# Kernel tuning notes

Measured on AMD Instinct MI355X. Metric: run time of the kernel, lower is better.

Reference implementation:

```python
import jax, jax.numpy as jnp
import numpy as np

NUM_HEADS = 3
DIM = 96
MLP_HIDDEN = int(DIM * 4.0)
LN_EPS = 1e-5


def _layernorm(x, g, b):
    mu = jnp.mean(x, axis=-1, keepdims=True)
    var = jnp.mean(jnp.square(x - mu), axis=-1, keepdims=True)
    return (x - mu) * jax.lax.rsqrt(var + LN_EPS) * g + b


def setup_inputs() -> dict:
    key = jax.random.key(0)
    ks = jax.random.split(key, 12)
    B, H, W, T, C = 1, 48, 48, 48, DIM
    L = H * W * T
    s = 0.02
    return {
        "x": jax.random.normal(ks[0], (B, L, C), dtype=jnp.float32),
        "mask_matrix": jnp.zeros((1, 1), dtype=jnp.float32),
        "ln1_g": jnp.ones((C,), jnp.float32),
        "ln1_b": jnp.zeros((C,), jnp.float32),
        "qkv_w": jax.random.normal(ks[1], (3 * C, C), jnp.float32) * s,
        "qkv_b": jnp.zeros((3 * C,), jnp.float32),
        "proj_w": jax.random.normal(ks[2], (C, C), jnp.float32) * s,
        "proj_b": jnp.zeros((C,), jnp.float32),
        "ln2_g": jnp.ones((C,), jnp.float32),
        "ln2_b": jnp.zeros((C,), jnp.float32),
        "fc1_w": jax.random.normal(ks[3], (MLP_HIDDEN, C), jnp.float32) * s,
        "fc1_b": jnp.zeros((MLP_HIDDEN,), jnp.float32),
        "fc2_w": jax.random.normal(ks[4], (C, MLP_HIDDEN), jnp.float32) * s,
        "fc2_b": jnp.zeros((C,), jnp.float32),
        "H": 48, "W": 48, "T": 48,
    }


def reference(x, mask_matrix, ln1_g, ln1_b, qkv_w, qkv_b, proj_w, proj_b,
              ln2_g, ln2_b, fc1_w, fc1_b, fc2_w, fc2_b, H, W, T):
    B, L, C = x.shape
    nh = NUM_HEADS
    hd = C // nh
    scale = hd ** -0.5

    shortcut = x
    h = _layernorm(x, ln1_g, ln1_b)
    # [B,H,W,T,C] -> permute(0,3,1,2,4) -> [B*T, H*W, C]  (axial_dims='12', extra_dim=3)
    h = h.reshape(B, H, W, T, C).transpose(0, 3, 1, 2, 4).reshape(B * T, H * W, C)
    B_, N, _ = h.shape

    qkv = h @ qkv_w.T + qkv_b                       # [B_, N, 3C]
    # faithful to torch: permute(1,0,2) -> reshape(1,N,3,nh,B_*hd) -> permute(2,0,3,1,4)
    qkv = jnp.transpose(qkv, (1, 0, 2)).reshape(1, N, 3, nh, B_ * hd)
    qkv = jnp.transpose(qkv, (2, 0, 3, 1, 4))       # [3, 1, nh, N, B_*hd]
    q, k, v = qkv[0] * scale, qkv[1], qkv[2]

    attn = jax.nn.softmax(q @ jnp.swapaxes(k, -2, -1), axis=-1)  # [1, nh, N, N]
    o = attn @ v                                    # [1, nh, N, B_*hd]
    o = jnp.transpose(o, (0, 2, 1, 3)).reshape(B_, N, C)
    o = o @ proj_w.T + proj_b
    # faithful to torch: plain view back to [B, H*W*T, C] (no inverse permute)
    o = o.reshape(B, H * W * T, C)

    x = shortcut + o
    h2 = _layernorm(x, ln2_g, ln2_b)
    m = jax.nn.gelu(h2 @ fc1_w.T + fc1_b, approximate=False) @ fc2_w.T + fc2_b
    return x + m
```

## Files before the change

### kernel.cpp

```cpp
#include <hip/hip_runtime.h>
#include <hip/hip_bf16.h>
#include <math.h>

typedef __bf16 bf16_t;
typedef __bf16 bf16x8 __attribute__((ext_vector_type(8)));
typedef __bf16 bf16x4 __attribute__((ext_vector_type(4)));
typedef float f32x4 __attribute__((ext_vector_type(4)));

#define AS1q __attribute__((address_space(1)))
#define AS3q __attribute__((address_space(3)))

__device__ __forceinline__ void gload_lds16(const bf16_t* g, bf16_t* l) {
    __builtin_amdgcn_global_load_lds((AS1q void*)g, (AS3q void*)l, 16, 0, 0);
}

#define LROWS   110592
#define CDIM    96
#define NTOK    2304
#define FDIM    1536
#define YSTR    3538944ll
#define SSTR    5308416ll
#define SCALE_Q 0.1767766952966369f

__device__ __forceinline__ float gelu_f(float v) {
    float xs = v * 0.70710678118654752f;
    float a  = fabsf(xs);
    float t  = __builtin_amdgcn_rcpf(fmaf(0.3275911f, a, 1.0f));
    float p  = t * fmaf(t, fmaf(t, fmaf(t, fmaf(t, 1.061405429f, -1.453152027f),
                                        1.421413741f), -0.284496736f), 0.254829592f);
    float e  = __expf(-a * a);
    float erfx = copysignf(fmaf(-p, e, 1.0f), xs);
    return 0.5f * v * (1.0f + erfx);
}

__global__ __launch_bounds__(256)
void conv_w(const float* __restrict__ a, const float* __restrict__ b,
            const float* __restrict__ c, const float* __restrict__ d,
            bf16_t* __restrict__ out)
{
    int i = blockIdx.x * 256 + threadIdx.x;
    float v;
    if (i < 27648)       v = a[i];
    else if (i < 36864)  v = b[i - 27648];
    else if (i < 73728)  v = c[i - 36864];
    else                 v = d[i - 73728];
    out[i] = (bf16_t)v;
}

__global__ __launch_bounds__(256)
void ln4_kernel(const float* __restrict__ x, const float* __restrict__ gamma,
                const float* __restrict__ beta, bf16_t* __restrict__ out, int permute)
{
    int wave = threadIdx.x >> 6;
    int half = (threadIdx.x >> 5) & 1;
    int cl   = threadIdx.x & 31;
    int row  = blockIdx.x * 8 + wave * 2 + half;
    bool act = cl < 24;
    const f32x4* xr = (const f32x4*)(x + (size_t)row * CDIM);
    f32x4 v = {0.f, 0.f, 0.f, 0.f};
    if (act) v = xr[cl];
    float s = v[0] + v[1] + v[2] + v[3];
    #pragma unroll
    for (int off = 16; off > 0; off >>= 1) s += __shfl_xor(s, off, 64);
    float mean = s * (1.f / 96.f);
    f32x4 d = {0.f, 0.f, 0.f, 0.f};
    if (act) { d[0]=v[0]-mean; d[1]=v[1]-mean; d[2]=v[2]-mean; d[3]=v[3]-mean; }
    float vs = d[0]*d[0] + d[1]*d[1] + d[2]*d[2] + d[3]*d[3];
    #pragma unroll
    for (int off = 16; off > 0; off >>= 1) vs += __shfl_xor(vs, off, 64);
    float rstd = rsqrtf(vs * (1.f / 96.f) + 1e-5f);
    size_t orow = row;
    if (permute) { int t = row % 48; int n = row / 48; orow = (size_t)t * NTOK + n; }
    if (act) {
        f32x4 g = ((const f32x4*)gamma)[cl];
        f32x4 b = ((const f32x4*)beta)[cl];
        bf16x4 o;
        #pragma unroll
        for (int j = 0; j < 4; j++) o[j] = (bf16_t)(d[j] * rstd * g[j] + b[j]);
        *(bf16x4*)(out + orow * CDIM + cl * 4) = o;
    }
}

__global__ __launch_bounds__(256)
void softmax_k(const bf16_t* __restrict__ S, bf16_t* __restrict__ P,
               long long sZ, long long pZ)
{
    int wv = threadIdx.x >> 6, lane = threadIdx.x & 63;
    int row = blockIdx.x * 4 + wv;
    const bf16_t* sr = S + (size_t)blockIdx.z * sZ + (size_t)row * NTOK;
    bf16_t* pr = P + (size_t)blockIdx.z * pZ + (size_t)row * NTOK;
    float v[36];
    float mx = -1e30f;
    #pragma unroll
    for (int t = 0; t < 9; t++) {
        bf16x4 c = *(const bf16x4*)(sr + (size_t)(t * 64 + lane) * 4);
        #pragma unroll
        for (int j = 0; j < 4; j++) { v[t*4+j] = (float)c[j]; mx = fmaxf(mx, v[t*4+j]); }
    }
    #pragma unroll
    for (int off = 32; off > 0; off >>= 1) mx = fmaxf(mx, __shfl_xor(mx, off, 64));
    float sum = 0.f;
    #pragma unroll
    for (int j = 0; j < 36; j++) { v[j] = __expf(v[j] - mx); sum += v[j]; }
    #pragma unroll
    for (int off = 32; off > 0; off >>= 1) sum += __shfl_xor(sum, off, 64);
    float inv = 1.f / sum;
    #pragma unroll
    for (int t = 0; t < 9; t++) {
        bf16x4 o;
        #pragma unroll
        for (int j = 0; j < 4; j++) o[j] = (bf16_t)(v[t*4+j] * inv);
        *(bf16x4*)(pr + (size_t)(t * 64 + lane) * 4) = o;
    }
}

template<int BN, int EPI, int NBY>
__global__ __launch_bounds__(256, 2)
void gemm_bt(const bf16_t* __restrict__ A, const bf16_t* __restrict__ W,
             void* __restrict__ out, int K,
             long long aZ, long long wZ, long long oZ, float scale)
{
    constexpr int BM = 128, BK = 64;
    constexpr int MI = 4;
    constexpr int NT = BN / 32;
    constexpr int NB = 18 * NBY;
    constexpr int CHK = (NB + 7) / 8;
    __shared__ bf16_t As[2][BM * BK];
    __shared__ bf16_t Bs[2][BN * BK];

    int id = blockIdx.x;
    int id2 = (id & 7) * CHK + (id >> 3);
    if (id2 >= NB) return;
    int p  = id2 / 108;
    int r_ = id2 - p * 108;
    int by = p * 6 + (r_ % 6);
    int bx = r_ / 6;

    const int tid = threadIdx.x;
    const int wave = tid >> 6, lane = tid & 63;
    const int quad = lane >> 4, l16 = lane & 15;
    const int wm = wave & 1, wn = wave >> 1;
    const int z = blockIdx.z;
    A += (size_t)z * aZ;
    W += (size_t)z * wZ;
    const int m0 = bx * BM, n0 = by * BN;

    f32x4 acc[MI][NT];
    #pragma unroll
    for (int i = 0; i < MI; i++)
        #pragma unroll
        for (int j = 0; j < NT; j++) { f32x4 zz = {0.f, 0.f, 0.f, 0.f}; acc[i][j] = zz; }

    const int srow = lane >> 3;
    const int scol = lane & 7;

    auto stage = [&](int buf, int k0) {
        for (int it = wave; it < BM / 8; it += 4) {
            int r = it * 8 + srow;
            int cg = scol ^ (r & 7);
            gload_lds16(A + (size_t)(m0 + r) * K + k0 + cg * 8, &As[buf][it * 512]);
        }
        for (int it = wave; it < BN / 8; it += 4) {
            int r = it * 8 + srow;
            int cg = scol ^ (r & 7);
            gload_lds16(W + (size_t)(n0 + r) * K + k0 + cg * 8, &Bs[buf][it * 512]);
        }
    };

    stage(0, 0);
    __syncthreads();

    int cur = 0;
    for (int k0 = 0; k0 < K; k0 += BK) {
        if (k0 + BK < K) stage(cur ^ 1, k0 + BK);

        bf16x8 af[MI][2], bfr[NT][2];
        #pragma unroll
        for (int i = 0; i < MI; i++) {
            int r = wm * 64 + i * 16 + l16;
            #pragma unroll
            for (int kk = 0; kk < 2; kk++)
                af[i][kk] = *(const bf16x8*)&As[cur][r * 64 + (((kk * 4 + quad) ^ (r & 7)) << 3)];
        }
        #pragma unroll
        for (int j = 0; j < NT; j++) {
            int c = wn * (BN / 2) + j * 16 + l16;
            #pragma unroll
            for (int kk = 0; kk < 2; kk++)
                bfr[j][kk] = *(const bf16x8*)&Bs[cur][c * 64 + (((kk * 4 + quad) ^ (c & 7)) << 3)];
        }
        #pragma unroll
        for (int kk = 0; kk < 2; kk++)
            #pragma unroll
            for (int i = 0; i < MI; i++)
                #pragma unroll
                for (int j = 0; j < NT; j++)
                    acc[i][j] = __builtin_amdgcn_mfma_f32_16x16x32_bf16(af[i][kk], bfr[j][kk], acc[i][j], 0, 0, 0);

        __syncthreads();
        cur ^= 1;
    }

    #pragma unroll
    for (int i = 0; i < MI; i++)
        #pragma unroll
        for (int j = 0; j < NT; j++)
            #pragma unroll
            for (int ri = 0; ri < 4; ri++) {
                int r = m0 + wm * 64 + i * 16 + quad * 4 + ri;
                int c = n0 + wn * (BN / 2) + j * 16 + l16;
                float v = acc[i][j][ri];
                if constexpr (EPI == 1) {
                    bf16_t* op = (bf16_t*)out + (size_t)z * oZ;
                    op[(size_t)r * NTOK + c] = (bf16_t)(v * scale);
                } else {
                    int b = r / 48, rr = r - b * 48;
                    ((bf16_t*)out)[((size_t)(b * NTOK + rr * 48 + z * 16)) * CDIM + c] = (bf16_t)v;
                }
            }
}

template<int N, int K, int KC, int EPI>
__global__ __launch_bounds__(256, 2)
void gemm_ws(const bf16_t* __restrict__ A, const bf16_t* __restrict__ Wg,
             void* __restrict__ out, const float* __restrict__ bias,
             const float* __restrict__ resid,
             bf16_t* __restrict__ out2, const float* __restrict__ g2,
             const float* __restrict__ b2)
{
    constexpr int KP = K + 8;
    constexpr int NT = N / 16;
    constexpr int KI = KC / 32;
    __shared__ __attribute__((aligned(16))) bf16_t Ws[N * KP];

    const int tid = threadIdx.x;
    const int wave = tid >> 6, lane = tid & 63;
    const int quad = lane >> 4, l16 = lane & 15;
    const int m0 = blockIdx.x * 256;

    constexpr int CH = N * K / 8;
    for (int c = tid; c < CH; c += 256) {
        int row = c / (K / 8), kc = c - row * (K / 8);
        bf16x8 w = *(const bf16x8*)(Wg + row * K + kc * 8);
        *(bf16x8*)(Ws + row * KP + kc * 8) = w;
    }
    __syncthreads();

    const bf16_t* Ar = A + (size_t)(m0 + wave * 64 + l16) * K + quad * 8;

    const int t = m0 / NTOK;
    const int nb = m0 - t * NTOK;

    auto epi_tile = [&](int nt, const f32x4* a4) {
        int c = nt * 16 + l16;
        if constexpr (EPI == 0) {
            int jj = t * 288 + c;
            int g = jj / FDIM, mm = jj - g * FDIM;
            float bv = bias[c];
            if (g < 6) {
                bf16_t* yp = (bf16_t*)out + (size_t)g * YSTR + mm;
                #pragma unroll
                for (int i = 0; i < 4; i++)
                    #pragma unroll
                    for (int ri = 0; ri < 4; ri++) {
                        int n = nb + wave * 64 + i * 16 + quad * 4 + ri;
                        yp[(size_t)n * FDIM] = (bf16_t)(a4[i][ri] + bv);
                    }
            } else {
                bf16_t* vp = out2 + (size_t)(g - 6) * YSTR + (size_t)mm * NTOK;
                #pragma unroll
                for (int i = 0; i < 4; i++) {
                    int n0q = nb + wave * 64 + i * 16 + quad * 4;
                    bf16x4 o;
                    #pragma unroll
                    for (int ri = 0; ri < 4; ri++) o[ri] = (bf16_t)(a4[i][ri] + bv);
                    *(bf16x4*)(vp + n0q) = o;
                }
            }
        } else {
            float bv = bias[c];
            #pragma unroll
            for (int i = 0; i < 4; i++)
                #pragma unroll
                for (int ri = 0; ri < 4; ri++) {
                    int r = m0 + wave * 64 + i * 16 + quad * 4 + ri;
                    float v = a4[i][ri] + bv;
                    if constexpr (EPI == 3) {
                        v = gelu_f(v);
                        ((bf16_t*)out)[(size_t)r * N + c] = (bf16_t)v;
                    } else {
                        ((float*)out)[(size_t)r * N + c] = v + resid[(size_t)r * N + c];
                    }
                }
        }
    };

    if constexpr (KC == K && EPI != 5) {
        bf16x8 af[4][KI];
        #pragma unroll
        for (int i = 0; i < 4; i++)
            #pragma unroll
            for (int kk = 0; kk < KI; kk++)
                af[i][kk] = *(const bf16x8*)(Ar + (size_t)i * 16 * K + kk * 32);
        #pragma unroll 2
        for (int nt = 0; nt < NT; nt++) {
            bf16x8 bfr[KI];
            #pragma unroll
            for (int kk = 0; kk < KI; kk++)
                bfr[kk] = *(const bf16x8*)(Ws + (nt * 16 + l16) * KP + kk * 32 + quad * 8);
            f32x4 a4[4];
            #pragma unroll
            for (int i = 0; i < 4; i++) { f32x4 zz = {0.f, 0.f, 0.f, 0.f}; a4[i] = zz; }
            #pragma unroll
            for (int kk = 0; kk < KI; kk++)
                #pragma unroll
                for (int i = 0; i < 4; i++)
                    a4[i] = __builtin_amdgcn_mfma_f32_16x16x32_bf16(af[i][kk], bfr[kk], a4[i], 0, 0, 0);
            epi_tile(nt, a4);
        }
    } else {
        f32x4 acc[4][NT];
        #pragma unroll
        for (int i = 0; i < 4; i++)
            #pragma unroll
            for (int j = 0; j < NT; j++) { f32x4 zz = {0.f, 0.f, 0.f, 0.f}; acc[i][j] = zz; }
        for (int kc0 = 0; kc0 < K; kc0 += KC) {
            bf16x8 af[4][KI];
            #pragma unroll
            for (int i = 0; i < 4; i++)
                #pragma unroll
                for (int kk = 0; kk < KI; kk++)
                    af[i][kk] = *(const bf16x8*)(Ar + (size_t)i * 16 * K + kc0 + kk * 32);
            #pragma unroll
            for (int nt = 0; nt < NT; nt++) {
                #pragma unroll
                for (int kk = 0; kk < KI; kk++) {
                    bf16x8 b = *(const bf16x8*)(Ws + (nt * 16 + l16) * KP + kc0 + kk * 32 + quad * 8);
                    #pragma unroll
                    for (int i = 0; i < 4; i++)
                        acc[i][nt] = __builtin_amdgcn_mfma_f32_16x16x32_bf16(af[i][kk], b, acc[i][nt], 0, 0, 0);
                }
            }
        }
        if constexpr (EPI == 5) {
            float bv[NT], gv[NT], bb[NT];
            #pragma unroll
            for (int nt = 0; nt < NT; nt++) {
                int c = nt * 16 + l16;
                bv[nt] = bias[c]; gv[nt] = g2[c]; bb[nt] = b2[c];
            }
            #pragma unroll
            for (int i = 0; i < 4; i++)
                #pragma unroll
                for (int ri = 0; ri < 4; ri++) {
                    int r = m0 + wave * 64 + i * 16 + quad * 4 + ri;
                    float u[NT];
                    float s = 0.f;
                    #pragma unroll
                    for (int nt = 0; nt < NT; nt++) {
                        int c = nt * 16 + l16;
                        u[nt] = acc[i][nt][ri] + bv[nt] + resid[(size_t)r * N + c];
                        ((float*)out)[(size_t)r * N + c] = u[nt];
                        s += u[nt];
                    }
                    #pragma unroll
                    for (int off = 8; off > 0; off >>= 1) s += __shfl_xor(s, off, 64);
                    float mean = s * (1.f / 96.f);
                    float vs = 0.f;
                    #pragma unroll
                    for (int nt = 0; nt < NT; nt++) {
                        float dd = u[nt] - mean;
                        u[nt] = dd;
                        vs += dd * dd;
                    }
                    #pragma unroll
                    for (int off = 8; off > 0; off >>= 1) vs += __shfl_xor(vs, off, 64);
                    float rstd = rsqrtf(vs * (1.f / 96.f) + 1e-5f);
                    #pragma unroll
                    for (int nt = 0; nt < NT; nt++) {
                        int c = nt * 16 + l16;
                        out2[(size_t)r * N + c] = (bf16_t)(u[nt] * rstd * gv[nt] + bb[nt]);
                    }
                }
        } else {
            #pragma unroll
            for (int nt = 0; nt < NT; nt++) {
                f32x4 a4[4];
                #pragma unroll
                for (int i = 0; i < 4; i++) a4[i] = acc[i][nt];
                epi_tile(nt, a4);
            }
        }
    }
}

__global__ __launch_bounds__(256, 4)
void mlp_fused(const bf16_t* __restrict__ A, const bf16_t* __restrict__ W1g,
               const bf16_t* __restrict__ W2g, const float* __restrict__ b1,
               const float* __restrict__ b2, const float* __restrict__ resid,
               float* __restrict__ out)
{
    constexpr int KP1 = 104;
    __shared__ __attribute__((aligned(16))) bf16_t W1c[2][32 * KP1];
    __shared__ __attribute__((aligned(16))) bf16_t W2c[2][96 * 40];
    __shared__ __attribute__((aligned(16))) bf16_t Tb[128 * 40];

    const int tid = threadIdx.x;
    const int wave = tid >> 6, lane = tid & 63;
    const int quad = lane >> 4, l16 = lane & 15;
    const int m0 = blockIdx.x * 128;

    const bf16_t* Ar = A + (size_t)(m0 + wave * 32 + l16) * 96 + quad * 8;
    bf16x8 af[2][3];
    #pragma unroll
    for (int i = 0; i < 2; i++)
        #pragma unroll
        for (int kk = 0; kk < 3; kk++)
            af[i][kk] = *(const bf16x8*)(Ar + (size_t)i * 16 * 96 + kk * 32);

    bf16x4 w1n[3], w2n[3];
    #pragma unroll
    for (int q = 0; q < 3; q++) {
        int e = q * 256 + tid;
        w1n[q] = *(const bf16x4*)(W1g + e * 4);
        int row = e >> 3, sub = e & 7;
        w2n[q] = *(const bf16x4*)(W2g + row * 384 + sub * 4);
    }
    #pragma unroll
    for (int q = 0; q < 3; q++) {
        int e = q * 256 + tid;
        int r1 = e / 24, s1 = e - r1 * 24;
        *(bf16x4*)(&W1c[0][r1 * KP1 + s1 * 4]) = w1n[q];
        int row = e >> 3, sub = e & 7;
        *(bf16x4*)(&W2c[0][row * 40 + sub * 4]) = w2n[q];
    }
    __syncthreads();

    f32x4 acc2[2][6];
    #pragma unroll
    for (int i = 0; i < 2; i++)
        #pragma unroll
        for (int j = 0; j < 6; j++) { f32x4 zz = {0.f, 0.f, 0.f, 0.f}; acc2[i][j] = zz; }

    for (int c = 0; c < 12; c++) {
        const int pb = c & 1;
        if (c < 11) {
            #pragma unroll
            for (int q = 0; q < 3; q++) {
                int e = q * 256 + tid;
                w1n[q] = *(const bf16x4*)(W1g + (c + 1) * 3072 + e * 4);
                int row = e >> 3, sub = e & 7;
                w2n[q] = *(const bf16x4*)(W2g + row * 384 + (c + 1) * 32 + sub * 4);
            }
        }
        f32x4 a1[2][2];
        #pragma unroll
        for (int i = 0; i < 2; i++)
            #pragma unroll
            for (int s = 0; s < 2; s++) { f32x4 zz = {0.f, 0.f, 0.f, 0.f}; a1[i][s] = zz; }
        #pragma unroll
        for (int s = 0; s < 2; s++) {
            int n = s * 16 + l16;
            #pragma unroll
            for (int kk = 0; kk < 3; kk++) {
                bf16x8 b = *(const bf16x8*)(&W1c[pb][n * KP1 + kk * 32 + quad * 8]);
                #pragma unroll
                for (int i = 0; i < 2; i++)
                    a1[i][s] = __builtin_amdgcn_mfma_f32_16x16x32_bf16(af[i][kk], b, a1[i][s], 0, 0, 0);
            }
        }
        #pragma unroll
        for (int s = 0; s < 2; s++) {
            int n = c * 32 + s * 16 + l16;
            float bv = b1[n];
            #pragma unroll
            for (int i = 0; i < 2; i++)
                #pragma unroll
                for (int ri = 0; ri < 4; ri++) {
                    float u = gelu_f(a1[i][s][ri] + bv);
                    Tb[(wave * 32 + i * 16 + quad * 4 + ri) * 40 + s * 16 + l16] = (bf16_t)u;
                }
        }
        if (c < 11) {
            #pragma unroll
            for (int q = 0; q < 3; q++) {
                int e = q * 256 + tid;
                int r1 = e / 24, s1 = e - r1 * 24;
                *(bf16x4*)(&W1c[pb ^ 1][r1 * KP1 + s1 * 4]) = w1n[q];
                int row = e >> 3, sub = e & 7;
                *(bf16x4*)(&W2c[pb ^ 1][row * 40 + sub * 4]) = w2n[q];
            }
        }
        bf16x8 a2[2];
        #pragma unroll
        for (int i = 0; i < 2; i++)
            a2[i] = *(const bf16x8*)(Tb + (wave * 32 + i * 16 + l16) * 40 + quad * 8);
        #pragma unroll
        for (int nt = 0; nt < 6; nt++) {
            bf16x8 b = *(const bf16x8*)(&W2c[pb][(nt * 16 + l16) * 40 + quad * 8]);
            #pragma unroll
            for (int i = 0; i < 2; i++)
                acc2[i][nt] = __builtin_amdgcn_mfma_f32_16x16x32_bf16(a2[i], b, acc2[i][nt], 0, 0, 0);
        }
        __syncthreads();
    }

    #pragma unroll
    for (int i = 0; i < 2; i++)
        #pragma unroll
        for (int nt = 0; nt < 6; nt++)
            #pragma unroll
            for (int ri = 0; ri < 4; ri++) {
                int r = m0 + wave * 32 + i * 16 + quad * 4 + ri;
                int cc = nt * 16 + l16;
                out[(size_t)r * 96 + cc] = acc2[i][nt][ri] + b2[cc] + resid[(size_t)r * 96 + cc];
            }
}

extern "C" void kernel_launch(void* const* d_in, const int* in_sizes, int n_in,
                              void* d_out, int out_size, void* d_ws, size_t ws_size,
                              hipStream_t stream)
{
    const float* x      = (const float*)d_in[0];
    const float* ln1_g  = (const float*)d_in[2];
    const float* ln1_b  = (const float*)d_in[3];
    const float* qkv_w  = (const float*)d_in[4];
    const float* qkv_b  = (const float*)d_in[5];
    const float* proj_w = (const float*)d_in[6];
    const float* proj_b = (const float*)d_in[7];
    const float* ln2_g  = (const float*)d_in[8];
    const float* ln2_b  = (const float*)d_in[9];
    const float* fc1_w  = (const float*)d_in[10];
    const float* fc1_b  = (const float*)d_in[11];
    const float* fc2_w  = (const float*)d_in[12];
    const float* fc2_b  = (const float*)d_in[13];

    const size_t SZ_WB = 110592ull * 2;
    const size_t SZ_HP = 10616832ull * 2;
    const size_t SZ_Y  = 31850496ull * 2;
    const size_t SZ_YV = 10616832ull * 2;

    char* ws = (char*)d_ws;
    size_t oWB = 0;
    size_t oHP = oWB + SZ_WB;
    size_t oY  = oHP + SZ_HP;
    size_t oYV = oY + SZ_Y;
    size_t oS  = oYV + SZ_YV;

    bf16_t* Wb    = (bf16_t*)(ws + oWB);
    bf16_t* Wqkv  = Wb;
    bf16_t* Wproj = Wb + 27648;
    bf16_t* Wfc1  = Wb + 36864;
    bf16_t* Wfc2  = Wb + 73728;
    bf16_t* hp    = (bf16_t*)(ws + oHP);
    bf16_t* Y     = (bf16_t*)(ws + oY);
    bf16_t* Yv    = (bf16_t*)(ws + oYV);
    bf16_t* Pb    = (bf16_t*)(ws + oY);
    bf16_t* Sb    = (bf16_t*)(ws + oS);
    float*  x2    = (float*)(ws + oS);
    float*  outp  = (float*)d_out;

    dim3 blk(256);

    conv_w<<<dim3(432), blk, 0, stream>>>(qkv_w, proj_w, fc1_w, fc2_w, Wb);
    ln4_kernel<<<dim3(13824), blk, 0, stream>>>(x, ln1_g, ln1_b, hp, 1);
    gemm_ws<288, 96, 96, 0><<<dim3(432), blk, 0, stream>>>(hp, Wqkv, Y, qkv_b,
                                                           nullptr, Yv, nullptr, nullptr);
    gemm_bt<128, 1, 18><<<dim3(328, 1, 3), blk, 0, stream>>>(Y, Y + 3 * YSTR, Sb,
                                                             1536, YSTR, YSTR, SSTR, SCALE_Q);
    softmax_k<<<dim3(576, 1, 3), blk, 0, stream>>>(Sb, Pb, SSTR, SSTR);
    gemm_bt<128, 2, 12><<<dim3(216, 1, 3), blk, 0, stream>>>(Pb, Yv, hp,
                                                             2304, SSTR, YSTR, 0, 0.f);
    gemm_ws<96, 96, 96, 5><<<dim3(432), blk, 0, stream>>>(hp, Wproj, x2, proj_b, x,
                                                          hp, ln2_g, ln2_b);
    mlp_fused<<<dim3(864), blk, 0, stream>>>(hp, Wfc1, Wfc2, fc1_b, fc2_b, x2, outp);
}
```

Measured before the change: 386.4 us.

## Replace attention GEMMs with 256x256-tile, 512-thread double-buffered pipelined kernel

Replaces the 128-row-tile attention GEMM (QK^T and PV) with a 256x256 tile kernel using 8 waves. Each wave now computes a 128x64 sub-tile, which raises reuse of data loaded into LDS. Global-to-LDS loads are issued two tiles ahead and tracked with explicit vmcnt waits and raw barriers, and s_setprio is raised around the MFMA section. Block IDs are remapped so that contiguous work is grouped per XCD. The larger tiles mean fewer blocks (243 and 162 in total) and heavier register use, which may reduce occupancy and leave part of the device idle.

After: 364.4 us. -5.7%, faster.

```diff
diff --git a/kernel.cpp b/kernel.cpp
--- a/kernel.cpp
+++ b/kernel.cpp
@@ -114,101 +114,122 @@
     }
 }
 
-template<int BN, int EPI, int NBY>
-__global__ __launch_bounds__(256, 2)
-void gemm_bt(const bf16_t* __restrict__ A, const bf16_t* __restrict__ W,
-             void* __restrict__ out, int K,
-             long long aZ, long long wZ, long long oZ, float scale)
-{
-    constexpr int BM = 128, BK = 64;
-    constexpr int MI = 4;
-    constexpr int NT = BN / 32;
-    constexpr int NB = 18 * NBY;
-    constexpr int CHK = (NB + 7) / 8;
-    __shared__ bf16_t As[2][BM * BK];
-    __shared__ bf16_t Bs[2][BN * BK];
-
-    int id = blockIdx.x;
-    int id2 = (id & 7) * CHK + (id >> 3);
-    if (id2 >= NB) return;
-    int p  = id2 / 108;
-    int r_ = id2 - p * 108;
-    int by = p * 6 + (r_ % 6);
-    int bx = r_ / 6;
+template<int EPI>
+__global__ __launch_bounds__(512, 1)
+void gemm_bt2(const bf16_t* __restrict__ A, const bf16_t* __restrict__ W,
+              void* __restrict__ out, int K,
+              long long aZ, long long wZ, long long oZ, float scale)
+{
+    constexpr int BM = 256, BN = 256, BK = 64;
+    __shared__ __attribute__((aligned(16))) bf16_t As[2][BM * BK];
+    __shared__ __attribute__((aligned(16))) bf16_t Bs[2][BN * BK];
+
+    const int nb = gridDim.x;
+    const int orig = blockIdx.x;
+    const int q8 = nb >> 3, r8 = nb & 7;
+    const int xcd = orig & 7;
+    const int wgid = (xcd < r8 ? xcd * (q8 + 1) : r8 * (q8 + 1) + (xcd - r8) * q8)
+                   + (orig >> 3);
+    const int bx = wgid % 9;
+    const int by = wgid / 9;
 
     const int tid = threadIdx.x;
     const int wave = tid >> 6, lane = tid & 63;
     const int quad = lane >> 4, l16 = lane & 15;
-    const int wm = wave & 1, wn = wave >> 1;
+    const int wm = wave >> 2, wn = wave & 3;
     const int z = blockIdx.z;
     A += (size_t)z * aZ;
     W += (size_t)z * wZ;
     const int m0 = bx * BM, n0 = by * BN;
 
-    f32x4 acc[MI][NT];
-    #pragma unroll
-    for (int i = 0; i < MI; i++)
-        #pragma unroll
-        for (int j = 0; j < NT; j++) { f32x4 zz = {0.f, 0.f, 0.f, 0.f}; acc[i][j] = zz; }
+    f32x4 acc[8][4];
+    #pragma unroll
+    for (int i = 0; i < 8; i++)
+        #pragma unroll
+        for (int j = 0; j < 4; j++) { f32x4 zz = {0.f, 0.f, 0.f, 0.f}; acc[i][j] = zz; }
 
     const int srow = lane >> 3;
     const int scol = lane & 7;
 
     auto stage = [&](int buf, int k0) {
-        for (int it = wave; it < BM / 8; it += 4) {
+        #pragma unroll
+        for (int it2 = 0; it2 < 4; it2++) {
+            int it = it2 * 8 + wave;
             int r = it * 8 + srow;
             int cg = scol ^ (r & 7);
             gload_lds16(A + (size_t)(m0 + r) * K + k0 + cg * 8, &As[buf][it * 512]);
         }
-        for (int it = wave; it < BN / 8; it += 4) {
+        #pragma unroll
+        for (int it2 = 0; it2 < 4; it2++) {
+            int it = it2 * 8 + wave;
             int r = it * 8 + srow;
             int cg = scol ^ (r & 7);
             gload_lds16(W + (size_t)(n0 + r) * K + k0 + cg * 8, &Bs[buf][it * 512]);
         }
     };
 
+    auto compute_tile = [&](int cb) {
+        #pragma unroll
+        for (int kk = 0; kk < 2; kk++) {
+            bf16x8 bfr[4];
+            #pragma unroll
+            for (int j = 0; j < 4; j++) {
+                int c = wn * 64 + j * 16 + l16;
+                bfr[j] = *(const bf16x8*)&Bs[cb][c * 64 + (((kk * 4 + quad) ^ (c & 7)) << 3)];
+            }
+            #pragma unroll
+            for (int ih = 0; ih < 2; ih++) {
+                bf16x8 af[4];
+                #pragma unroll
+                for (int i = 0; i < 4; i++) {
+                    int r = wm * 128 + (ih * 4 + i) * 16 + l16;
+                    af[i] = *(const bf16x8*)&As[cb][r * 64 + (((kk * 4 + quad) ^ (r & 7)) << 3)];
+                }
+                #pragma unroll
+                for (int i = 0; i < 4; i++)
+                    #pragma unroll
+                    for (int j = 0; j < 4; j++)
+                        acc[ih * 4 + i][j] = __builtin_amdgcn_mfma_f32_16x16x32_bf16(
+                            af[i], bfr[j], acc[ih * 4 + i][j], 0, 0, 0);
+            }
+        }
+    };
+
+    const int nt = K / BK;
+
     stage(0, 0);
-    __syncthreads();
+    stage(1, BK);
 
     int cur = 0;
-    for (int k0 = 0; k0 < K; k0 += BK) {
-        if (k0 + BK < K) stage(cur ^ 1, k0 + BK);
-
-        bf16x8 af[MI][2], bfr[NT][2];
-        #pragma unroll
-        for (int i = 0; i < MI; i++) {
-            int r = wm * 64 + i * 16 + l16;
-            #pragma unroll
-            for (int kk = 0; kk < 2; kk++)
-                af[i][kk] = *(const bf16x8*)&As[cur][r * 64 + (((kk * 4 + quad) ^ (r & 7)) << 3)];
-        }
-        #pragma unroll
-        for (int j = 0; j < NT; j++) {
-            int c = wn * (BN / 2) + j * 16 + l16;
-            #pragma unroll
-            for (int kk = 0; kk < 2; kk++)
-                bfr[j][kk] = *(const bf16x8*)&Bs[cur][c * 64 + (((kk * 4 + quad) ^ (c & 7)) << 3)];
-        }
-        #pragma unroll
-        for (int kk = 0; kk < 2; kk++)
-            #pragma unroll
-            for (int i = 0; i < MI; i++)
-                #pragma unroll
-                for (int j = 0; j < NT; j++)
-                    acc[i][j] = __builtin_amdgcn_mfma_f32_16x16x32_bf16(af[i][kk], bfr[j][kk], acc[i][j], 0, 0, 0);
-
-        __syncthreads();
+    for (int kt = 0; kt < nt - 1; kt++) {
+        asm volatile("s_waitcnt vmcnt(8)" ::: "memory");
+        __builtin_amdgcn_sched_barrier(0);
+        __builtin_amdgcn_s_barrier();
+        __builtin_amdgcn_sched_barrier(0);
+        __builtin_amdgcn_s_setprio(1);
+        compute_tile(cur);
+        __builtin_amdgcn_s_setprio(0);
+        asm volatile("s_waitcnt lgkmcnt(0)" ::: "memory");
+        __builtin_amdgcn_sched_barrier(0);
+        __builtin_amdgcn_s_barrier();
+        __builtin_amdgcn_sched_barrier(0);
+        if (kt + 2 < nt) stage(cur, (kt + 2) * BK);
         cur ^= 1;
     }
-
-    #pragma unroll
-    for (int i = 0; i < MI; i++)
-        #pragma unroll
-        for (int j = 0; j < NT; j++)
+    asm volatile("s_waitcnt vmcnt(0)" ::: "memory");
+    __builtin_amdgcn_sched_barrier(0);
+    __builtin_amdgcn_s_barrier();
+    __builtin_amdgcn_sched_barrier(0);
+    compute_tile(cur);
+
+    #pragma unroll
+    for (int i = 0; i < 8; i++)
+        #pragma unroll
+        for (int j = 0; j < 4; j++)
             #pragma unroll
             for (int ri = 0; ri < 4; ri++) {
-                int r = m0 + wm * 64 + i * 16 + quad * 4 + ri;
-                int c = n0 + wn * (BN / 2) + j * 16 + l16;
+                int r = m0 + wm * 128 + i * 16 + quad * 4 + ri;
+                int c = n0 + wn * 64 + j * 16 + l16;
                 float v = acc[i][j][ri];
                 if constexpr (EPI == 1) {
                     bf16_t* op = (bf16_t*)out + (size_t)z * oZ;
@@ -566,11 +587,11 @@
     ln4_kernel<<<dim3(13824), blk, 0, stream>>>(x, ln1_g, ln1_b, hp, 1);
     gemm_ws<288, 96, 96, 0><<<dim3(432), blk, 0, stream>>>(hp, Wqkv, Y, qkv_b,
                                                            nullptr, Yv, nullptr, nullptr);
-    gemm_bt<128, 1, 18><<<dim3(328, 1, 3), blk, 0, stream>>>(Y, Y + 3 * YSTR, Sb,
-                                                             1536, YSTR, YSTR, SSTR, SCALE_Q);
+    gemm_bt2<1><<<dim3(81, 1, 3), dim3(512), 0, stream>>>(Y, Y + 3 * YSTR, Sb,
+                                                          1536, YSTR, YSTR, SSTR, SCALE_Q);
     softmax_k<<<dim3(576, 1, 3), blk, 0, stream>>>(Sb, Pb, SSTR, SSTR);
-    gemm_bt<128, 2, 12><<<dim3(216, 1, 3), blk, 0, stream>>>(Pb, Yv, hp,
-                                                             2304, SSTR, YSTR, 0, 0.f);
+    gemm_bt2<2><<<dim3(54, 1, 3), dim3(512), 0, stream>>>(Pb, Yv, hp,
+                                                          2304, SSTR, YSTR, 0, 0.f);
     gemm_ws<96, 96, 96, 5><<<dim3(432), blk, 0, stream>>>(hp, Wproj, x2, proj_b, x,
                                                           hp, ln2_g, ln2_b);
     mlp_fused<<<dim3(864), blk, 0, stream>>>(hp, Wfc1, Wfc2, fc1_b, fc2_b, x2, outp);
```
